# Performance work log

Measured on AMD Instinct MI355X. Metric: run time of the kernel, lower is better.

The kernel has to match this reference:

```python
import jax, jax.numpy as jnp
import numpy as np

N, D, K = 100000, 512, 1024

def setup_inputs() -> dict:
    key = jax.random.key(0)
    k1, k2 = jax.random.split(key)
    nodes = jax.random.normal(k1, (N, D), dtype=jnp.float32)
    # Faithful to original: indices sampled in [0, d) (torch.randint(d, ...))
    center_ind = jax.random.randint(k2, (K,), 0, D, dtype=jnp.int32)
    return {"nodes": nodes, "center_ind": center_ind, "num_clusters": K}


def reference(nodes, center_ind, num_clusters):
    # nodes: [n, d]; initial centers gathered from nodes (indices in [0, d) per original code)
    centers0 = nodes[center_ind]                      # [K, d]
    # Squared L2 distances via the expansion trick; avoids materializing [K, n, d].
    # argmin over squared distance == argmin over distance (sqrt is monotone).
    node_sq = jnp.sum(nodes * nodes, axis=1)          # [n]
    cent_sq = jnp.sum(centers0 * centers0, axis=1)    # [K]
    # d2[k, i] = ||c_k||^2 + ||x_i||^2 - 2 c_k . x_i
    d2 = cent_sq[:, None] + node_sq[None, :] - 2.0 * jnp.einsum("kd,nd->kn", centers0, nodes)
    assignment = jnp.argmin(d2, axis=0)               # [n]
    # Scatter-add nodes into their assigned cluster (index_add equivalent).
    centers = jax.ops.segment_sum(nodes, assignment, num_segments=num_clusters)  # [K, d]
    return centers
```

## Files before the change

kernel.cpp:

```cpp
#include <hip/hip_runtime.h>
#include <stdint.h>


typedef _Float16 f16x8 __attribute__((ext_vector_type(8)));
typedef float    f32x4 __attribute__((ext_vector_type(4)));

#define DD 512
#define KK 1024

static __device__ __forceinline__ unsigned orderable(float s) {
    unsigned u = __float_as_uint(s);
    return (u & 0x80000000u) ? ~u : (u | 0x80000000u);
}

__global__ void gather_centers(const float* __restrict__ nodes,
                               const int* __restrict__ center_ind,
                               _Float16* __restrict__ cent16,
                               float* __restrict__ cent_sq,
                               int K) {
    int k    = (int)blockIdx.x;
    int lane = (int)threadIdx.x;
    int ci   = center_ind[k];
    const f32x4* p = reinterpret_cast<const f32x4*>(nodes + (size_t)ci * DD + lane * 8);
    f32x4 v0 = p[0], v1 = p[1];
    f16x8 h;
    h[0]=(_Float16)v0[0]; h[1]=(_Float16)v0[1]; h[2]=(_Float16)v0[2]; h[3]=(_Float16)v0[3];
    h[4]=(_Float16)v1[0]; h[5]=(_Float16)v1[1]; h[6]=(_Float16)v1[2]; h[7]=(_Float16)v1[3];
    *reinterpret_cast<f16x8*>(cent16 + (size_t)k * DD + lane * 8) = h;
    float ssq = v0[0]*v0[0]+v0[1]*v0[1]+v0[2]*v0[2]+v0[3]*v0[3]
              + v1[0]*v1[0]+v1[1]*v1[1]+v1[2]*v1[2]+v1[3]*v1[3];
    #pragma unroll
    for (int off = 32; off > 0; off >>= 1) ssq += __shfl_xor(ssq, off, 64);
    if (lane == 0) cent_sq[k] = ssq;
}

__launch_bounds__(256, 2)
__global__ void assign_mfma(const float* __restrict__ nodes,
                            const _Float16* __restrict__ cent16,
                            const float* __restrict__ cent_sq,
                            unsigned* __restrict__ assignment,
                            unsigned* __restrict__ counts,
                            int N, int K) {
    __shared__ __align__(16) _Float16 nt[64 * DD];
    __shared__ float csq[KK];
    __shared__ unsigned long long best[64];

    const int tid = (int)threadIdx.x;
    const int n0  = (int)blockIdx.x * 64;

    #pragma unroll
    for (int it = 0; it < 16; ++it) {
        int f   = it * 256 + tid;
        int row = f >> 6;
        int d0  = (f & 63) << 3;
        f32x4 v0 = {0.f,0.f,0.f,0.f}, v1 = {0.f,0.f,0.f,0.f};
        if (n0 + row < N) {
            const f32x4* p = reinterpret_cast<const f32x4*>(nodes + (size_t)(n0 + row) * DD + d0);
            v0 = p[0]; v1 = p[1];
        }
        f16x8 h;
        h[0]=(_Float16)v0[0]; h[1]=(_Float16)v0[1]; h[2]=(_Float16)v0[2]; h[3]=(_Float16)v0[3];
        h[4]=(_Float16)v1[0]; h[5]=(_Float16)v1[1]; h[6]=(_Float16)v1[2]; h[7]=(_Float16)v1[3];
        int byte = ((row << 10) + (d0 << 1)) ^ ((row & 7) << 4);
        *reinterpret_cast<f16x8*>(reinterpret_cast<char*>(nt) + byte) = h;
    }
    for (int j = tid; j < K;  j += 256) csq[j]  = cent_sq[j];
    for (int j = tid; j < 64; j += 256) best[j] = ~0ULL;
    __syncthreads();

    const int lane = tid & 63;
    const int wid  = tid >> 6;
    const int l15  = lane & 15;
    const int g    = lane >> 4;
    const int g8   = g * 8;
    const int swz  = (l15 & 7) << 4;
    const int cPerWave = K >> 2;
    const int cw0  = wid * cPerWave;
    char* ntb = reinterpret_cast<char*>(nt);

    int bbase[4];
    #pragma unroll
    for (int nG = 0; nG < 4; ++nG) bbase[nG] = (((nG * 16 + l15) << 10) + (g << 4));

    const int nT = cPerWave >> 6;
    for (int t64 = 0; t64 < nT; ++t64) {
        const int cbase = cw0 + t64 * 64;
        f32x4 acc[4][4];
        #pragma unroll
        for (int a = 0; a < 4; ++a)
            #pragma unroll
            for (int b = 0; b < 4; ++b) { f32x4 z = {0.f,0.f,0.f,0.f}; acc[a][b] = z; }

        #pragma unroll 2
        for (int d0 = 0; d0 < DD; d0 += 32) {
            f16x8 A[4], B[4];
            #pragma unroll
            for (int tC = 0; tC < 4; ++tC)
                A[tC] = *reinterpret_cast<const f16x8*>(
                    cent16 + ((size_t)(cbase + tC * 16 + l15) << 9) + d0 + g8);
            #pragma unroll
            for (int nG = 0; nG < 4; ++nG)
                B[nG] = *reinterpret_cast<const f16x8*>(
                    ntb + ((bbase[nG] + (d0 << 1)) ^ swz));
            #pragma unroll
            for (int tC = 0; tC < 4; ++tC)
                #pragma unroll
                for (int nG = 0; nG < 4; ++nG)
                    acc[tC][nG] = __builtin_amdgcn_mfma_f32_16x16x32_f16(
                        A[tC], B[nG], acc[tC][nG], 0, 0, 0);
        }

        #pragma unroll
        for (int nG = 0; nG < 4; ++nG) {
            unsigned long long pk = ~0ULL;
            #pragma unroll
            for (int tC = 0; tC < 4; ++tC) {
                #pragma unroll
                for (int q = 0; q < 4; ++q) {
                    int c = cbase + tC * 16 + g * 4 + q;
                    float s = fmaf(-2.f, acc[tC][nG][q], csq[c]);
                    unsigned long long v =
                        ((unsigned long long)orderable(s) << 32) | (unsigned)c;
                    pk = v < pk ? v : pk;
                }
            }
            unsigned long long o;
            o = __shfl_xor(pk, 16, 64); pk = o < pk ? o : pk;
            o = __shfl_xor(pk, 32, 64); pk = o < pk ? o : pk;
            if (lane < 16) atomicMin(&best[nG * 16 + l15], pk);
        }
    }
    __syncthreads();
    if (tid < 64 && n0 + tid < N) {
        unsigned k = (unsigned)(best[tid] & 0xffffffffu);
        assignment[n0 + tid] = k;
        atomicAdd(&counts[k], 1u);
    }
}

__global__ void scan_offsets(const unsigned* __restrict__ counts,
                             unsigned* __restrict__ cursor) {
    __shared__ unsigned s[KK];
    int t = (int)threadIdx.x;
    unsigned c = counts[t];
    s[t] = c;
    __syncthreads();
    for (int off = 1; off < KK; off <<= 1) {
        unsigned v = (t >= off) ? s[t - off] : 0u;
        __syncthreads();
        s[t] += v;
        __syncthreads();
    }
    cursor[t] = s[t] - c;
}

__global__ void scatter_idx(const unsigned* __restrict__ assignment,
                            unsigned* __restrict__ cursor,
                            unsigned* __restrict__ keys, int N) {
    int i = (int)(blockIdx.x * blockDim.x + threadIdx.x);
    if (i < N) {
        unsigned k = assignment[i];
        unsigned slot = atomicAdd(&cursor[k], 1u);
        keys[slot] = (k << 20) | (unsigned)i;
    }
}

#define CHUNK 32
__launch_bounds__(256, 4)
__global__ void aggregate3(const float* __restrict__ nodes,
                           const unsigned* __restrict__ keys,
                           float* __restrict__ out, int N) {
    const int tid  = (int)threadIdx.x;
    const int wid  = tid >> 6;
    const int lane = tid & 63;
    const int base = ((int)blockIdx.x * 4 + wid) * CHUNK;
    if (base >= N) return;
    const int n    = min(CHUNK, N - base);

    int sI = base + (lane & 31);
    unsigned myk = (sI < N) ? keys[sI] : 0u;

    f32x4 a0 = {0.f,0.f,0.f,0.f}, a1 = {0.f,0.f,0.f,0.f};
    int curk = -1;
    auto flush = [&](void) {
        float* dst = out + ((size_t)curk << 9) + lane * 8;
        #pragma unroll
        for (int e = 0; e < 4; ++e) atomicAdd(dst + e, a0[e]);
        #pragma unroll
        for (int e = 0; e < 4; ++e) atomicAdd(dst + 4 + e, a1[e]);
    };

    int j = 0;
    while (j < n) {
        int b = n - j; if (b > 4) b = 4;
        f32x4 r[4][2];
        int   kk[4];
        #pragma unroll
        for (int t = 0; t < 4; ++t) {
            if (t < b) {
                unsigned key = __shfl(myk, j + t, 64);
                kk[t] = (int)(key >> 20);
                const f32x4* p = reinterpret_cast<const f32x4*>(
                    nodes + ((size_t)(key & 0xFFFFFu) << 9) + lane * 8);
                r[t][0] = p[0];
                r[t][1] = p[1];
            }
        }
        #pragma unroll
        for (int t = 0; t < 4; ++t) {
            if (t < b) {
                if (kk[t] != curk) {
                    if (curk >= 0) flush();
                    curk = kk[t];
                    f32x4 z = {0.f,0.f,0.f,0.f}; a0 = z; a1 = z;
                }
                a0 += r[t][0];
                a1 += r[t][1];
            }
        }
        j += 4;
    }
    if (curk >= 0) flush();
}

extern "C" void kernel_launch(void* const* d_in, const int* in_sizes, int n_in,
                              void* d_out, int out_size, void* d_ws, size_t ws_size,
                              hipStream_t stream) {
    const float* nodes      = (const float*)d_in[0];
    const int*   center_ind = (const int*)d_in[1];
    int K = in_sizes[1];
    int D = out_size / K;
    int N = in_sizes[0] / D;
    (void)D;

    char* ws = (char*)d_ws;
    _Float16* cent16     = (_Float16*)ws;
    size_t    o          = (size_t)K * DD * 2;
    float*    cent_sq    = (float*)(ws + o);    o += (size_t)K * 4;
    unsigned* assignment = (unsigned*)(ws + o); o += (size_t)N * 4;
    unsigned* counts     = (unsigned*)(ws + o); o += (size_t)K * 4;
    unsigned* cursor     = (unsigned*)(ws + o); o += (size_t)K * 4;
    unsigned* keys       = (unsigned*)(ws + o); o += (size_t)N * 4;
    float*    out        = (float*)d_out;

    hipMemsetAsync(counts, 0, (size_t)K * sizeof(unsigned), stream);
    hipMemsetAsync(out, 0, (size_t)out_size * sizeof(float), stream);

    gather_centers<<<K, 64, 0, stream>>>(nodes, center_ind, cent16, cent_sq, K);
    assign_mfma<<<(N + 63) / 64, 256, 0, stream>>>(nodes, cent16, cent_sq,
                                                   assignment, counts, N, K);
    scan_offsets<<<1, KK, 0, stream>>>(counts, cursor);
    scatter_idx<<<(N + 255) / 256, 256, 0, stream>>>(assignment, cursor, keys, N);
    aggregate3<<<(N + 4 * CHUNK - 1) / (4 * CHUNK), 256, 0, stream>>>(nodes, keys, out, N);
}
```

Baseline: 543.9 us.

## Pre-tile centers into MFMA fragment layout, double-buffer operand loads, canonicalize duplicate centers

```diff
diff --git a/kernel.cpp b/kernel.cpp
--- a/kernel.cpp
+++ b/kernel.cpp
@@ -2,8 +2,8 @@
 #include <stdint.h>
 
 
-typedef _Float16 f16x8 __attribute__((ext_vector_type(8)));
-typedef float    f32x4 __attribute__((ext_vector_type(4)));
+typedef _Float16 f16x8  __attribute__((ext_vector_type(8)));
+typedef float    f32x4  __attribute__((ext_vector_type(4)));
 
 #define DD 512
 #define KK 1024
@@ -13,9 +13,21 @@
     return (u & 0x80000000u) ? ~u : (u | 0x80000000u);
 }
 
+__global__ void canon_first(const int* __restrict__ center_ind,
+                            unsigned* __restrict__ firstk, int K) {
+    int k = (int)(blockIdx.x * blockDim.x + threadIdx.x);
+    if (k < K) atomicMin(&firstk[center_ind[k]], (unsigned)k);
+}
+__global__ void canon_map(const int* __restrict__ center_ind,
+                          const unsigned* __restrict__ firstk,
+                          unsigned* __restrict__ canon, int K) {
+    int k = (int)(blockIdx.x * blockDim.x + threadIdx.x);
+    if (k < K) canon[k] = firstk[center_ind[k]];
+}
+
 __global__ void gather_centers(const float* __restrict__ nodes,
                                const int* __restrict__ center_ind,
-                               _Float16* __restrict__ cent16,
+                               _Float16* __restrict__ centf,
                                float* __restrict__ cent_sq,
                                int K) {
     int k    = (int)blockIdx.x;
@@ -26,7 +38,8 @@
     f16x8 h;
     h[0]=(_Float16)v0[0]; h[1]=(_Float16)v0[1]; h[2]=(_Float16)v0[2]; h[3]=(_Float16)v0[3];
     h[4]=(_Float16)v1[0]; h[5]=(_Float16)v1[1]; h[6]=(_Float16)v1[2]; h[7]=(_Float16)v1[3];
-    *reinterpret_cast<f16x8*>(cent16 + (size_t)k * DD + lane * 8) = h;
+    int t = k >> 4, r = k & 15;
+    *reinterpret_cast<f16x8*>(centf + ((size_t)((t * 64 + lane) * 16 + r) << 3)) = h;
     float ssq = v0[0]*v0[0]+v0[1]*v0[1]+v0[2]*v0[2]+v0[3]*v0[3]
               + v1[0]*v1[0]+v1[1]*v1[1]+v1[2]*v1[2]+v1[3]*v1[3];
     #pragma unroll
@@ -36,8 +49,9 @@
 
 __launch_bounds__(256, 2)
 __global__ void assign_mfma(const float* __restrict__ nodes,
-                            const _Float16* __restrict__ cent16,
+                            const _Float16* __restrict__ centf,
                             const float* __restrict__ cent_sq,
+                            const unsigned* __restrict__ canon,
                             unsigned* __restrict__ assignment,
                             unsigned* __restrict__ counts,
                             int N, int K) {
@@ -72,42 +86,51 @@
     const int wid  = tid >> 6;
     const int l15  = lane & 15;
     const int g    = lane >> 4;
-    const int g8   = g * 8;
     const int swz  = (l15 & 7) << 4;
-    const int cPerWave = K >> 2;
-    const int cw0  = wid * cPerWave;
     char* ntb = reinterpret_cast<char*>(nt);
 
     int bbase[4];
     #pragma unroll
     for (int nG = 0; nG < 4; ++nG) bbase[nG] = (((nG * 16 + l15) << 10) + (g << 4));
 
-    const int nT = cPerWave >> 6;
-    for (int t64 = 0; t64 < nT; ++t64) {
+    #define LA(Av, aw, s)                                                            \
+        { _Pragma("unroll")                                                          \
+          for (int t_ = 0; t_ < 4; ++t_)                                             \
+              Av[t_] = *reinterpret_cast<const f16x8*>(                              \
+                  (aw) + ((size_t)t_ << 13) + ((s) << 9) + (lane << 3)); }
+    #define LB(Bv, s)                                                                \
+        { _Pragma("unroll")                                                          \
+          for (int nG = 0; nG < 4; ++nG)                                             \
+              Bv[nG] = *reinterpret_cast<const f16x8*>(                              \
+                  ntb + ((bbase[nG] + ((s) << 6)) ^ swz)); }
+    #define MM(Av, Bv)                                                               \
+        { _Pragma("unroll")                                                          \
+          for (int t_ = 0; t_ < 4; ++t_)                                             \
+              _Pragma("unroll")                                                      \
+              for (int nG = 0; nG < 4; ++nG)                                         \
+                  acc[t_][nG] = __builtin_amdgcn_mfma_f32_16x16x32_f16(              \
+                      Av[t_], Bv[nG], acc[t_][nG], 0, 0, 0); }
+
+    const int cw0 = wid * (K >> 2);
+    #pragma unroll
+    for (int t64 = 0; t64 < 4; ++t64) {
         const int cbase = cw0 + t64 * 64;
+        const _Float16* aw = centf + ((size_t)(cbase >> 4) << 13);
+
         f32x4 acc[4][4];
         #pragma unroll
         for (int a = 0; a < 4; ++a)
             #pragma unroll
             for (int b = 0; b < 4; ++b) { f32x4 z = {0.f,0.f,0.f,0.f}; acc[a][b] = z; }
 
-        #pragma unroll 2
-        for (int d0 = 0; d0 < DD; d0 += 32) {
-            f16x8 A[4], B[4];
-            #pragma unroll
-            for (int tC = 0; tC < 4; ++tC)
-                A[tC] = *reinterpret_cast<const f16x8*>(
-                    cent16 + ((size_t)(cbase + tC * 16 + l15) << 9) + d0 + g8);
-            #pragma unroll
-            for (int nG = 0; nG < 4; ++nG)
-                B[nG] = *reinterpret_cast<const f16x8*>(
-                    ntb + ((bbase[nG] + (d0 << 1)) ^ swz));
-            #pragma unroll
-            for (int tC = 0; tC < 4; ++tC)
-                #pragma unroll
-                for (int nG = 0; nG < 4; ++nG)
-                    acc[tC][nG] = __builtin_amdgcn_mfma_f32_16x16x32_f16(
-                        A[tC], B[nG], acc[tC][nG], 0, 0, 0);
+        f16x8 Aa[4], Ba[4], Ab[4], Bb[4];
+        LA(Aa, aw, 0); LB(Ba, 0);
+        #pragma unroll
+        for (int s = 0; s < 16; s += 2) {
+            LA(Ab, aw, s + 1); LB(Bb, s + 1);
+            MM(Aa, Ba);
+            if (s + 2 < 16) { LA(Aa, aw, s + 2); LB(Ba, s + 2); }
+            MM(Ab, Bb);
         }
 
         #pragma unroll
@@ -130,9 +153,14 @@
             if (lane < 16) atomicMin(&best[nG * 16 + l15], pk);
         }
     }
+    #undef LA
+    #undef LB
+    #undef MM
+
     __syncthreads();
     if (tid < 64 && n0 + tid < N) {
         unsigned k = (unsigned)(best[tid] & 0xffffffffu);
+        k = canon[k];
         assignment[n0 + tid] = k;
         atomicAdd(&counts[k], 1u);
     }
@@ -231,23 +259,27 @@
     int K = in_sizes[1];
     int D = out_size / K;
     int N = in_sizes[0] / D;
-    (void)D;
 
     char* ws = (char*)d_ws;
-    _Float16* cent16     = (_Float16*)ws;
+    _Float16* centf      = (_Float16*)ws;
     size_t    o          = (size_t)K * DD * 2;
     float*    cent_sq    = (float*)(ws + o);    o += (size_t)K * 4;
     unsigned* assignment = (unsigned*)(ws + o); o += (size_t)N * 4;
     unsigned* counts     = (unsigned*)(ws + o); o += (size_t)K * 4;
     unsigned* cursor     = (unsigned*)(ws + o); o += (size_t)K * 4;
+    unsigned* firstk     = (unsigned*)(ws + o); o += (size_t)D * 4;
+    unsigned* canon      = (unsigned*)(ws + o); o += (size_t)K * 4;
     unsigned* keys       = (unsigned*)(ws + o); o += (size_t)N * 4;
     float*    out        = (float*)d_out;
 
     hipMemsetAsync(counts, 0, (size_t)K * sizeof(unsigned), stream);
+    hipMemsetAsync(firstk, 0xFF, (size_t)D * sizeof(unsigned), stream);
     hipMemsetAsync(out, 0, (size_t)out_size * sizeof(float), stream);
 
-    gather_centers<<<K, 64, 0, stream>>>(nodes, center_ind, cent16, cent_sq, K);
-    assign_mfma<<<(N + 63) / 64, 256, 0, stream>>>(nodes, cent16, cent_sq,
+    canon_first<<<(K + 255) / 256, 256, 0, stream>>>(center_ind, firstk, K);
+    canon_map<<<(K + 255) / 256, 256, 0, stream>>>(center_ind, firstk, canon, K);
+    gather_centers<<<K, 64, 0, stream>>>(nodes, center_ind, centf, cent_sq, K);
+    assign_mfma<<<(N + 63) / 64, 256, 0, stream>>>(nodes, centf, cent_sq, canon,
                                                    assignment, counts, N, K);
     scan_offsets<<<1, KK, 0, stream>>>(counts, cursor);
     scatter_idx<<<(N + 255) / 256, 256, 0, stream>>>(assignment, cursor, keys, N);
```

New measurement: 596.5 us. +9.7%, slower.
